# Optimization experiments

Measured on AMD Instinct MI355X. Metric: run time of the kernel, lower is better.

## Reference

```python
import jax, jax.numpy as jnp
import numpy as np

B, T, DIN, DOUT = 32, 3136, 192, 384
H, QS, WS = 6, 4, 16            # heads, q_stride, window_size (post-pool)
HD = DOUT // H                   # head_dim = 64
INNER = QS * WS                  # tokens per mask unit before pooling = 64
NW = T // INNER                  # num_windows = 49
MLP_HID = 4 * DOUT
EPS = 1e-5


def layer_norm(x, w, b):
    mu = x.mean(-1, keepdims=True)
    var = ((x - mu) ** 2).mean(-1, keepdims=True)
    return (x - mu) * jax.lax.rsqrt(var + EPS) * w + b


def setup_inputs() -> dict:
    key = jax.random.key(0)
    ks = jax.random.split(key, 16)
    rn = lambda k, shp, fan: jax.random.normal(k, shp, jnp.float32) * (fan ** -0.5)
    return {
        "embeddings": jax.random.normal(ks[0], (B, T, DIN), jnp.float32),
        "norm1_w": jnp.ones((DIN,), jnp.float32),
        "norm1_b": jnp.zeros((DIN,), jnp.float32),
        "w_qkv": rn(ks[1], (3 * DOUT, DIN), DIN),
        "b_qkv": jnp.zeros((3 * DOUT,), jnp.float32),
        "w_attn_proj": rn(ks[2], (DOUT, DOUT), DOUT),
        "b_attn_proj": jnp.zeros((DOUT,), jnp.float32),
        "w_res_proj": rn(ks[3], (DOUT, DIN), DIN),
        "b_res_proj": jnp.zeros((DOUT,), jnp.float32),
        "norm2_w": jnp.ones((DOUT,), jnp.float32),
        "norm2_b": jnp.zeros((DOUT,), jnp.float32),
        "w_fc1": rn(ks[4], (MLP_HID, DOUT), DOUT),
        "b_fc1": jnp.zeros((MLP_HID,), jnp.float32),
        "w_fc2": rn(ks[5], (DOUT, MLP_HID), MLP_HID),
        "b_fc2": jnp.zeros((DOUT,), jnp.float32),
    }


def _block(embeddings, norm1_w, norm1_b, w_qkv, b_qkv, w_attn_proj, b_attn_proj,
           w_res_proj, b_res_proj, norm2_w, norm2_b, w_fc1, b_fc1, w_fc2, b_fc2):
    x = layer_norm(embeddings, norm1_w, norm1_b)                 # [B,T,DIN]

    # residual path: project then do_pool (max over q_stride groups)
    res = x @ w_res_proj.T + b_res_proj                          # [B,T,DOUT]
    res = res.reshape(B, QS, T // QS, DOUT).max(axis=1)          # [B,T/QS,DOUT]

    # mask-unit attention
    qkv = x @ w_qkv.T + b_qkv                                    # [B,T,3*DOUT]
    qkv = qkv.reshape(B, INNER, NW, 3, H, HD)
    qkv = jnp.transpose(qkv, (3, 0, 4, 2, 1, 5))                 # [3,B,H,NW,INNER,HD]
    q, k, v = qkv[0], qkv[1], qkv[2]
    q = q.reshape(B, H, NW, QS, WS, HD).max(axis=3)              # q-pool -> [B,H,NW,WS,HD]
    scale = HD ** -0.5
    attn = jax.nn.softmax(jnp.einsum("bhwqd,bhwkd->bhwqk", q * scale, k), axis=-1)
    out = jnp.einsum("bhwqk,bhwkd->bhwqd", attn, v)              # [B,H,NW,WS,HD]
    out = jnp.transpose(out, (0, 3, 2, 1, 4)).reshape(B, WS * NW, DOUT)
    out = out @ w_attn_proj.T + b_attn_proj

    emb = res + out
    h = layer_norm(emb, norm2_w, norm2_b)
    h = jax.nn.gelu(h @ w_fc1.T + b_fc1, approximate=False)
    emb = emb + (h @ w_fc2.T + b_fc2)
    return emb, attn


def reference(embeddings, norm1_w, norm1_b, w_qkv, b_qkv, w_attn_proj, b_attn_proj,
              w_res_proj, b_res_proj, norm2_w, norm2_b, w_fc1, b_fc1, w_fc2, b_fc2):
    return _block(embeddings, norm1_w, norm1_b, w_qkv, b_qkv, w_attn_proj, b_attn_proj,
                  w_res_proj, b_res_proj, norm2_w, norm2_b, w_fc1, b_fc1, w_fc2, b_fc2)
```

## Files before the change

### kernel.cpp

```cpp
#include <hip/hip_runtime.h>
#include <stdint.h>

typedef __bf16 bf16_t;
typedef __attribute__((ext_vector_type(8))) __bf16 bf16x8;
typedef __attribute__((ext_vector_type(4))) __bf16 bf16x4;
typedef __attribute__((ext_vector_type(4))) float f32x4;

#define NB_ 32
#define NT_ 3136
#define DIN_ 192
#define DOUT_ 384
#define NH_ 6
#define HD_ 64
#define NW_ 49
#define WSZ_ 16
#define TP_ 784
#define MLP_ 1536

__device__ __forceinline__ f32x4 mfma16(bf16x8 a, bf16x8 b, f32x4 c) {
  return __builtin_amdgcn_mfma_f32_16x16x32_bf16(a, b, c, 0, 0, 0);
}

__device__ __forceinline__ void gload_lds16(const bf16_t* g, bf16_t* l) {
  __builtin_amdgcn_global_load_lds(
      (const __attribute__((address_space(1))) void*)((const void*)g),
      (__attribute__((address_space(3))) void*)l, 16, 0, 0);
}

__device__ __forceinline__ float gelu_tanh(float v) {
  const float t2 = 1.5957691216f * (v + 0.044715f * v * v * v);
  return v * (1.f - 1.f / (1.f + __expf(t2)));
}

__global__ void cvt_kernel(const float* __restrict__ s0, const float* __restrict__ s1,
                           const float* __restrict__ s2, const float* __restrict__ s3,
                           const float* __restrict__ s4, bf16_t* __restrict__ d0,
                           bf16_t* __restrict__ d1, bf16_t* __restrict__ d2,
                           bf16_t* __restrict__ d3, bf16_t* __restrict__ d4) {
  const int b = blockIdx.x;
  const float* s; bf16_t* d; long off;
  if (b < 108)      { s = s0; d = d0; off = (long)b * 2048; }
  else if (b < 144) { s = s1; d = d1; off = (long)(b - 108) * 2048; }
  else if (b < 216) { s = s2; d = d2; off = (long)(b - 144) * 2048; }
  else if (b < 504) { s = s3; d = d3; off = (long)(b - 216) * 2048; }
  else              { s = s4; d = d4; off = (long)(b - 504) * 2048; }
  off += (long)threadIdx.x * 8;
  const float4 a = *(const float4*)(s + off);
  const float4 c = *(const float4*)(s + off + 4);
  bf16x8 o;
  o[0] = (bf16_t)a.x; o[1] = (bf16_t)a.y; o[2] = (bf16_t)a.z; o[3] = (bf16_t)a.w;
  o[4] = (bf16_t)c.x; o[5] = (bf16_t)c.y; o[6] = (bf16_t)c.z; o[7] = (bf16_t)c.w;
  *(bf16x8*)(d + off) = o;
}

template <int D>
__global__ void ln_f32_kernel(const float* __restrict__ in, const float* __restrict__ w,
                              const float* __restrict__ bvec, bf16_t* __restrict__ out) {
  const int row = blockIdx.x * 4 + (threadIdx.x >> 6);
  const int lane = threadIdx.x & 63;
  constexpr int PER = D / 64;
  const float* x = in + (long)row * D;
  float v[PER];
  float s = 0.f;
#pragma unroll
  for (int i = 0; i < PER; i++) { v[i] = x[lane * PER + i]; s += v[i]; }
#pragma unroll
  for (int off = 1; off < 64; off <<= 1) s += __shfl_xor(s, off);
  const float mu = s * (1.f / D);
  float s2 = 0.f;
#pragma unroll
  for (int i = 0; i < PER; i++) { const float d = v[i] - mu; s2 += d * d; }
#pragma unroll
  for (int off = 1; off < 64; off <<= 1) s2 += __shfl_xor(s2, off);
  const float rstd = rsqrtf(s2 * (1.f / D) + 1e-5f);
  bf16_t* o = out + (long)row * D;
#pragma unroll
  for (int i = 0; i < PER; i++) {
    const int c = lane * PER + i;
    o[c] = (bf16_t)((v[i] - mu) * rstd * w[c] + bvec[c]);
  }
}

template <int D>
__global__ void ln_bf16_kernel(const bf16_t* __restrict__ in, const float* __restrict__ w,
                               const float* __restrict__ bvec, bf16_t* __restrict__ out) {
  const int row = blockIdx.x * 4 + (threadIdx.x >> 6);
  const int lane = threadIdx.x & 63;
  constexpr int PER = D / 64;
  const bf16_t* x = in + (long)row * D;
  float v[PER];
  float s = 0.f;
#pragma unroll
  for (int i = 0; i < PER; i++) { v[i] = (float)x[lane * PER + i]; s += v[i]; }
#pragma unroll
  for (int off = 1; off < 64; off <<= 1) s += __shfl_xor(s, off);
  const float mu = s * (1.f / D);
  float s2 = 0.f;
#pragma unroll
  for (int i = 0; i < PER; i++) { const float d = v[i] - mu; s2 += d * d; }
#pragma unroll
  for (int off = 1; off < 64; off <<= 1) s2 += __shfl_xor(s2, off);
  const float rstd = rsqrtf(s2 * (1.f / D) + 1e-5f);
  bf16_t* o = out + (long)row * D;
#pragma unroll
  for (int i = 0; i < PER; i++) {
    const int c = lane * PER + i;
    o[c] = (bf16_t)((v[i] - mu) * rstd * w[c] + bvec[c]);
  }
}

template <int ACT, int POOL>
__global__ __launch_bounds__(512, 4) void gemm8(
    const bf16_t* __restrict__ A, const bf16_t* __restrict__ W,
    const float* __restrict__ bias, bf16_t* __restrict__ C,
    int M, int N, int K) {
  __shared__ __align__(16) char AsB[256 * 128];
  __shared__ __align__(16) char WsB[128 * 128];

  const int nwg = gridDim.x;
  const int q = nwg >> 3, rm = nwg & 7;
  const int xcd = blockIdx.x & 7, idx = blockIdx.x >> 3;
  const int wg = (xcd < rm ? xcd * (q + 1) : rm * (q + 1) + (xcd - rm) * q) + idx;

  const int nbn = N >> 7;
  const int bmi = wg / nbn;
  const int bni = wg - bmi * nbn;
  const int m0 = bmi << 8, n0 = bni << 7;
  const int tid = threadIdx.x;
  const int lane = tid & 63;
  const int wid = tid >> 6;
  const int wr = (wid >> 1) * 64, wc = (wid & 1) * 64;
  const int l15 = lane & 15;
  const int lkb = (lane >> 4) << 4;
  const int srow = tid >> 3;
  const int scolsw = ((tid & 7) << 3) ^ ((srow & 7) << 3);
  const int swzr = (l15 & 7) << 4;

  f32x4 acc[4][4];
  const f32x4 zero = {0.f, 0.f, 0.f, 0.f};
#pragma unroll
  for (int i = 0; i < 4; i++)
#pragma unroll
    for (int j = 0; j < 4; j++) acc[i][j] = zero;

  long arow[4];
#pragma unroll
  for (int p = 0; p < 4; p++) {
    const int m = m0 + p * 64 + srow;
    if constexpr (POOL) {
      const int b = m / NT_;
      const int mm = m - b * NT_;
      arow[p] = (long)b * NT_ + (mm & 3) * TP_ + (mm >> 2);
    } else {
      arow[p] = m;
    }
  }
  long wrow[2];
#pragma unroll
  for (int p = 0; p < 2; p++) wrow[p] = (long)(n0 + p * 64 + srow);

  for (int k0 = 0; k0 < K; k0 += 64) {
    __syncthreads();
#pragma unroll
    for (int p = 0; p < 4; p++)
      gload_lds16(A + arow[p] * K + k0 + scolsw, (bf16_t*)(AsB + p * 8192 + tid * 16));
#pragma unroll
    for (int p = 0; p < 2; p++)
      gload_lds16(W + wrow[p] * K + k0 + scolsw, (bf16_t*)(WsB + p * 8192 + tid * 16));
    __syncthreads();
#pragma unroll
    for (int kk = 0; kk < 2; kk++) {
      bf16x8 af[4], wf[4];
#pragma unroll
      for (int i = 0; i < 4; i++)
        af[i] = *(const bf16x8*)(AsB + (wr + i * 16 + l15) * 128 + ((kk * 64 + lkb) ^ swzr));
#pragma unroll
      for (int j = 0; j < 4; j++)
        wf[j] = *(const bf16x8*)(WsB + (wc + j * 16 + l15) * 128 + ((kk * 64 + lkb) ^ swzr));
#pragma unroll
      for (int i = 0; i < 4; i++)
#pragma unroll
        for (int j = 0; j < 4; j++) {
          if constexpr (POOL) acc[i][j] = mfma16(af[i], wf[j], acc[i][j]);
          else                acc[i][j] = mfma16(wf[j], af[i], acc[i][j]);
        }
    }
  }

  const int rg = (lane >> 4) * 4;
  if constexpr (POOL) {
#pragma unroll
    for (int j = 0; j < 4; j++) {
      const int gn = n0 + wc + j * 16 + l15;
      const float bv = bias[gn];
#pragma unroll
      for (int i = 0; i < 4; i++) {
        const float v = fmaxf(fmaxf(acc[i][j][0], acc[i][j][1]),
                              fmaxf(acc[i][j][2], acc[i][j][3])) + bv;
        const long pm = (long)((m0 + wr + i * 16 + rg) >> 2);
        C[pm * N + gn] = (bf16_t)v;
      }
    }
  } else {
    __syncthreads();
    char* scr = AsB + wid * 4096;
#pragma unroll
    for (int i = 0; i < 4; i++) {
#pragma unroll
      for (int j = 0; j < 4; j++)
        *(f32x4*)(scr + l15 * 256 + ((((j * 16 + rg) << 2)) ^ ((l15 & 7) << 4))) = acc[i][j];
#pragma unroll
      for (int k = 0; k < 4; k++) {
        const int rl = k * 4 + (lane >> 4);
        const int cb = (lane & 15) << 4;
        const f32x4 v = *(const f32x4*)(scr + rl * 256 + (cb ^ ((rl & 7) << 4)));
        const long gm = m0 + wr + i * 16 + rl;
        const int gn = n0 + wc + ((lane & 15) << 2);
        const float4 bv = *(const float4*)(bias + gn);
        float vv[4] = {v[0] + bv.x, v[1] + bv.y, v[2] + bv.z, v[3] + bv.w};
        if constexpr (ACT == 1) {
#pragma unroll
          for (int r = 0; r < 4; r++) vv[r] = gelu_tanh(vv[r]);
        }
        bf16x4 o;
#pragma unroll
        for (int r = 0; r < 4; r++) o[r] = (bf16_t)vv[r];
        *(bf16x4*)(C + gm * N + gn) = o;
      }
    }
  }
}

template <int HASRES, int OF32, int RF32>
__global__ __launch_bounds__(256) void gemm_t(
    const bf16_t* __restrict__ A, const bf16_t* __restrict__ W,
    const float* __restrict__ bias, const void* __restrict__ resv,
    void* __restrict__ Cv, int M, int N, int K) {
  constexpr int BM = 64;
  constexpr int PA = BM / 32;
  constexpr int ABYTES = BM * 128;
  constexpr int BUFSZ = ABYTES + 128 * 128;
  __shared__ __align__(16) char LDSB[2 * BUFSZ];

  const int nwg = gridDim.x;
  const int q = nwg >> 3, rm = nwg & 7;
  const int xcd = blockIdx.x & 7, idx = blockIdx.x >> 3;
  const int wg = (xcd < rm ? xcd * (q + 1) : rm * (q + 1) + (xcd - rm) * q) + idx;

  const int nbn = N >> 7;
  const int bmi = wg / nbn;
  const int bni = wg - bmi * nbn;
  const int m0 = bmi * BM, n0 = bni << 7;
  const int tid = threadIdx.x;
  const int lane = tid & 63;
  const int wid = tid >> 6;
  const int wr = (wid >> 1) * 32, wc = (wid & 1) * 64;
  const int l15 = lane & 15;
  const int lkb = (lane >> 4) << 4;
  const int srow = tid >> 3;
  const int scolsw = ((tid & 7) << 3) ^ ((srow & 7) << 3);
  const int swzr = (l15 & 7) << 4;

  f32x4 acc[PA][4];
  const f32x4 zero = {0.f, 0.f, 0.f, 0.f};
#pragma unroll
  for (int i = 0; i < PA; i++)
#pragma unroll
    for (int j = 0; j < 4; j++) acc[i][j] = zero;

  long arow[PA];
#pragma unroll
  for (int p = 0; p < PA; p++) arow[p] = m0 + srow + p * 32;
  long wrow[4];
#pragma unroll
  for (int p = 0; p < 4; p++) wrow[p] = (long)(n0 + srow + p * 32);

  auto stage = [&](int buf, int k0) {
    char* base = LDSB + buf * BUFSZ;
#pragma unroll
    for (int p = 0; p < PA; p++)
      gload_lds16(A + arow[p] * K + k0 + scolsw, (bf16_t*)(base + p * 4096 + tid * 16));
#pragma unroll
    for (int p = 0; p < 4; p++)
      gload_lds16(W + wrow[p] * K + k0 + scolsw,
                  (bf16_t*)(base + ABYTES + p * 4096 + tid * 16));
  };

  const int nt = K >> 6;
  stage(0, 0);
  int cur = 0;
  for (int t = 0; t < nt; t++) {
    __syncthreads();
    if (t + 1 < nt) stage(cur ^ 1, (t + 1) << 6);
    const char* base = LDSB + cur * BUFSZ;
#pragma unroll
    for (int kk = 0; kk < 2; kk++) {
      bf16x8 af[PA], wf[4];
#pragma unroll
      for (int i = 0; i < PA; i++)
        af[i] = *(const bf16x8*)(base + (wr + i * 16 + l15) * 128 + ((kk * 64 + lkb) ^ swzr));
#pragma unroll
      for (int j = 0; j < 4; j++)
        wf[j] = *(const bf16x8*)(base + ABYTES + (wc + j * 16 + l15) * 128 +
                                 ((kk * 64 + lkb) ^ swzr));
#pragma unroll
      for (int i = 0; i < PA; i++)
#pragma unroll
        for (int j = 0; j < 4; j++) acc[i][j] = mfma16(wf[j], af[i], acc[i][j]);
    }
    cur ^= 1;
  }

  __syncthreads();
  char* scr = LDSB + wid * 8192;
  const int rg = (lane >> 4) * 4;
#pragma unroll
  for (int i = 0; i < PA; i++) {
    const int ml = i * 16 + l15;
#pragma unroll
    for (int j = 0; j < 4; j++)
      *(f32x4*)(scr + ml * 256 + ((((j * 16 + rg) << 2)) ^ ((ml & 7) << 4))) = acc[i][j];
  }
#pragma unroll
  for (int k = 0; k < 8; k++) {
    const int rl = k * 4 + (lane >> 4);
    const int cb = (lane & 15) << 4;
    const f32x4 v = *(const f32x4*)(scr + rl * 256 + (cb ^ ((rl & 7) << 4)));
    const long gm = m0 + wr + rl;
    const int gn = n0 + wc + ((lane & 15) << 2);
    const float4 bv = *(const float4*)(bias + gn);
    float vv[4] = {v[0] + bv.x, v[1] + bv.y, v[2] + bv.z, v[3] + bv.w};
    if constexpr (HASRES) {
      if constexpr (RF32) {
        const float4 rv = *(const float4*)((const float*)resv + gm * N + gn);
        vv[0] += rv.x; vv[1] += rv.y; vv[2] += rv.z; vv[3] += rv.w;
      } else {
        const bf16x4 rv = *(const bf16x4*)((const bf16_t*)resv + gm * N + gn);
#pragma unroll
        for (int r = 0; r < 4; r++) vv[r] += (float)rv[r];
      }
    }
    if constexpr (OF32) {
      float4 o = {vv[0], vv[1], vv[2], vv[3]};
      *(float4*)((float*)Cv + gm * N + gn) = o;
    } else {
      bf16x4 o;
#pragma unroll
      for (int r = 0; r < 4; r++) o[r] = (bf16_t)vv[r];
      *(bf16x4*)((bf16_t*)Cv + gm * N + gn) = o;
    }
  }
}

__global__ __launch_bounds__(384) void qkv_attn_kernel(
    const bf16_t* __restrict__ x, const bf16_t* __restrict__ Wqkv,
    const float* __restrict__ bq, float* __restrict__ prob,
    bf16_t* __restrict__ obuf) {
  __shared__ __align__(16) char As[64 * 384];
  __shared__ __align__(16) char Qs[6][2048];
  __shared__ __align__(16) char Kb[6][4096];
  const int b = blockIdx.x / NW_;
  const int w = blockIdx.x - b * NW_;
  const int tid = threadIdx.x;
  const int lane = tid & 63;
  const int h = tid >> 6;
  const int l15 = lane & 15;
  const int lk8 = (lane >> 4) * 8;
  const int lkb = (lane >> 4) << 4;
  const int rg = (lane >> 4) * 4;
  const f32x4 zero = {0.f, 0.f, 0.f, 0.f};

#pragma unroll
  for (int i = 0; i < 4; i++) {
    const int row = i * 16 + tid / 24;
    const int cb = ((tid % 24) * 16) ^ ((row & 7) << 4);
    gload_lds16(x + ((long)b * NT_ + (long)row * NW_ + w) * DIN_ + cb / 2,
                (bf16_t*)(As + i * 6144 + tid * 16));
  }
  __syncthreads();

  char* Qw = Qs[h];
  char* Bw = Kb[h];
  auto gemm_part = [&](int which, f32x4 (&acc)[4][4]) {
#pragma unroll
    for (int i = 0; i < 4; i++)
#pragma unroll
      for (int j = 0; j < 4; j++) acc[i][j] = zero;
#pragma unroll
    for (int j = 0; j < 4; j++) {
      const bf16_t* wrow = Wqkv + (long)(which * DOUT_ + h * HD_ + j * 16 + l15) * DIN_;
      bf16x8 wf[6];
#pragma unroll
      for (int ks = 0; ks < 6; ks++)
        wf[ks] = *(const bf16x8*)(wrow + ks * 32 + lk8);
#pragma unroll
      for (int ks = 0; ks < 6; ks++) {
#pragma unroll
        for (int i = 0; i < 4; i++) {
          const int mr = i * 16 + l15;
          const bf16x8 af = *(const bf16x8*)(As + mr * 384 +
                                             ((ks * 64 + lkb) ^ ((mr & 7) << 4)));
          acc[i][j] = mfma16(af, wf[ks], acc[i][j]);
        }
      }
    }
  };

  f32x4 acc[4][4];
  gemm_part(0, acc);
#pragma unroll
  for (int j = 0; j < 4; j++) {
    const float bb = bq[h * HD_ + j * 16 + l15];
#pragma unroll
    for (int r = 0; r < 4; r++) {
      const float v = (fmaxf(fmaxf(acc[0][j][r], acc[1][j][r]),
                             fmaxf(acc[2][j][r], acc[3][j][r])) + bb) * 0.125f;
      const int row = rg + r;
      *(bf16_t*)(Qw + row * 128 + (((j * 16 + l15) * 2) ^ ((row & 7) << 4))) = (bf16_t)v;
    }
  }
  bf16x8 aq[2];
#pragma unroll
  for (int kc = 0; kc < 2; kc++)
    aq[kc] = *(const bf16x8*)(Qw + l15 * 128 + ((kc * 64 + lkb) ^ ((l15 & 7) << 4)));

  gemm_part(1, acc);
#pragma unroll
  for (int j = 0; j < 4; j++) {
    const float bb = bq[DOUT_ + h * HD_ + j * 16 + l15];
#pragma unroll
    for (int i = 0; i < 4; i++)
#pragma unroll
      for (int r = 0; r < 4; r++) acc[i][j][r] += bb;
  }
  f32x4 s4[4];
#pragma unroll
  for (int nc = 0; nc < 4; nc++) s4[nc] = zero;
#pragma unroll
  for (int t = 0; t < 2; t++) {
#pragma unroll
    for (int i2 = 0; i2 < 2; i2++) {
      const int i = t * 2 + i2;
#pragma unroll
      for (int j = 0; j < 4; j++)
#pragma unroll
        for (int r = 0; r < 4; r++) {
          const int tokh = i2 * 16 + rg + r;
          *(bf16_t*)(Bw + tokh * 128 + (((j * 16 + l15) * 2) ^ ((tokh & 7) << 4))) =
              (bf16_t)acc[i][j][r];
        }
    }
#pragma unroll
    for (int nch = 0; nch < 2; nch++) {
      const int nc = t * 2 + nch;
      const int tokh = nch * 16 + l15;
#pragma unroll
      for (int kc = 0; kc < 2; kc++) {
        const bf16x8 bk = *(const bf16x8*)(Bw + tokh * 128 +
                                           ((kc * 64 + lkb) ^ ((tokh & 7) << 4)));
        s4[nc] = mfma16(aq[kc], bk, s4[nc]);
      }
    }
  }

#pragma unroll
  for (int r = 0; r < 4; r++) {
    float mx = fmaxf(fmaxf(s4[0][r], s4[1][r]), fmaxf(s4[2][r], s4[3][r]));
#pragma unroll
    for (int off = 1; off < 16; off <<= 1) mx = fmaxf(mx, __shfl_xor(mx, off));
    float sm = 0.f;
#pragma unroll
    for (int nc = 0; nc < 4; nc++) {
      const float p = __expf(s4[nc][r] - mx);
      s4[nc][r] = p;
      sm += p;
    }
#pragma unroll
    for (int off = 1; off < 16; off <<= 1) sm += __shfl_xor(sm, off);
    const float inv = 1.f / sm;
#pragma unroll
    for (int nc = 0; nc < 4; nc++) s4[nc][r] *= inv;
  }

  float* aout = prob + (long)((b * NH_ + h) * NW_ + w) * (WSZ_ * 64);
#pragma unroll
  for (int nc = 0; nc < 4; nc++) {
#pragma unroll
    for (int r = 0; r < 4; r++) {
      const int row = rg + r, col = nc * 16 + l15;
      aout[row * 64 + col] = s4[nc][r];
      *(bf16_t*)(Qw + row * 128 + ((col * 2) ^ ((row & 7) << 4))) = (bf16_t)s4[nc][r];
    }
  }
  bf16x8 ap[2];
#pragma unroll
  for (int kc = 0; kc < 2; kc++)
    ap[kc] = *(const bf16x8*)(Qw + l15 * 128 + ((kc * 64 + lkb) ^ ((l15 & 7) << 4)));

  gemm_part(2, acc);
#pragma unroll
  for (int j = 0; j < 4; j++) {
    const float bb = bq[2 * DOUT_ + h * HD_ + j * 16 + l15];
#pragma unroll
    for (int i = 0; i < 4; i++)
#pragma unroll
      for (int r = 0; r < 4; r++) acc[i][j][r] += bb;
  }
  f32x4 o4[4];
#pragma unroll
  for (int nc = 0; nc < 4; nc++) o4[nc] = zero;
#pragma unroll
  for (int t = 0; t < 2; t++) {
#pragma unroll
    for (int i2 = 0; i2 < 2; i2++) {
      const int i = t * 2 + i2;
#pragma unroll
      for (int j = 0; j < 4; j++)
#pragma unroll
        for (int r = 0; r < 4; r++) {
          const int tokh = i2 * 16 + rg + r;
          *(bf16_t*)(Bw + tokh * 128 + (((j * 16 + l15) * 2) ^ ((tokh & 7) << 4))) =
              (bf16_t)acc[i][j][r];
        }
    }
#pragma unroll
    for (int nc = 0; nc < 4; nc++) {
      bf16x8 bv;
#pragma unroll
      for (int e = 0; e < 8; e++) {
        const int tokh = lk8 + e;
        bv[e] = *(const bf16_t*)(Bw + tokh * 128 +
                                 (((nc * 16 + l15) * 2) ^ ((tokh & 7) << 4)));
      }
      o4[nc] = mfma16(ap[t], bv, o4[nc]);
    }
  }

#pragma unroll
  for (int nc = 0; nc < 4; nc++) {
#pragma unroll
    for (int r = 0; r < 4; r++) {
      const int row = rg + r;
      *(bf16_t*)(Qw + row * 128 + (((nc * 16 + l15) * 2) ^ ((row & 7) << 4))) =
          (bf16_t)o4[nc][r];
    }
  }
  bf16_t* ob = obuf + (long)b * TP_ * DOUT_ + h * HD_;
#pragma unroll
  for (int p = 0; p < 2; p++) {
    const int row = lane >> 2;
    const int cb = p * 64 + (lane & 3) * 16;
    const bf16x8 t = *(const bf16x8*)(Qw + row * 128 + (cb ^ ((row & 7) << 4)));
    *(bf16x8*)(ob + (long)(row * NW_ + w) * DOUT_ + cb / 2) = t;
  }
}

extern "C" void kernel_launch(void* const* d_in, const int* in_sizes, int n_in,
                              void* d_out, int out_size, void* d_ws, size_t ws_size,
                              hipStream_t stream) {
  const float* emb   = (const float*)d_in[0];
  const float* n1w   = (const float*)d_in[1];
  const float* n1b   = (const float*)d_in[2];
  const float* wqkv  = (const float*)d_in[3];
  const float* bqkv  = (const float*)d_in[4];
  const float* wproj = (const float*)d_in[5];
  const float* bproj = (const float*)d_in[6];
  const float* wres  = (const float*)d_in[7];
  const float* bres  = (const float*)d_in[8];
  const float* n2w   = (const float*)d_in[9];
  const float* n2b   = (const float*)d_in[10];
  const float* wfc1  = (const float*)d_in[11];
  const float* bfc1  = (const float*)d_in[12];
  const float* wfc2  = (const float*)d_in[13];
  const float* bfc2  = (const float*)d_in[14];
  float* out = (float*)d_out;

  const int BT = NB_ * NT_;
  const int BTP = NB_ * TP_;

  char* wsb = (char*)d_ws;
  bf16_t* x    = (bf16_t*)(wsb);
  bf16_t* h1   = (bf16_t*)(wsb);
  bf16_t* obuf = (bf16_t*)(wsb + 57802752L);
  bf16_t* resp = (bf16_t*)(wsb + 77070336L);
  bf16_t* h0   = resp;
  bf16_t* emb1 = (bf16_t*)(wsb + 96337920L);
  bf16_t* wbqkv = (bf16_t*)(wsb + 115605504L);
  bf16_t* wbres = wbqkv + 221184L;
  bf16_t* wbproj = wbres + 73728L;
  bf16_t* wbfc1 = wbproj + 147456L;
  bf16_t* wbfc2 = wbfc1 + 589824L;
  float*  prob = out + 9633792L;

  cvt_kernel<<<792, 256, 0, stream>>>(wqkv, wres, wproj, wfc1, wfc2,
                                      wbqkv, wbres, wbproj, wbfc1, wbfc2);
  ln_f32_kernel<DIN_><<<BT / 4, 256, 0, stream>>>(emb, n1w, n1b, x);
  gemm8<0, 1><<<(BT / 256) * (DOUT_ / 128), 512, 0, stream>>>(
      x, wbres, bres, resp, BT, DOUT_, DIN_);
  qkv_attn_kernel<<<NB_ * NW_, 384, 0, stream>>>(x, wbqkv, bqkv, prob, obuf);
  gemm_t<1, 0, 0><<<(BTP / 64) * (DOUT_ / 128), 256, 0, stream>>>(
      obuf, wbproj, bproj, resp, emb1, BTP, DOUT_, DOUT_);
  ln_bf16_kernel<DOUT_><<<BTP / 4, 256, 0, stream>>>(emb1, n2w, n2b, h0);
  gemm8<1, 0><<<(BTP / 256) * (MLP_ / 128), 512, 0, stream>>>(
      h0, wbfc1, bfc1, h1, BTP, MLP_, DOUT_);
  gemm_t<1, 1, 0><<<(BTP / 64) * (DOUT_ / 128), 256, 0, stream>>>(
      h1, wbfc2, bfc2, emb1, out, BTP, DOUT_, MLP_);
}
```

Before: 312.4 us.

## Process two batch elements per attention block to reuse QKV weight fragments

The fused QKV+attention kernel now handles two batch items per block for the same window. Each weight fragment loaded from global memory feeds MFMAs for both items, which halves weight traffic per output and halves the grid size. The cost is double the accumulator registers (acc0/acc1 of 16 f32x4 each), larger LDS (about 96KB per block), and a launch-bounds hint of 2 blocks per CU that may force spills. The smaller grid of 784 blocks also lowers parallelism.

```diff
diff --git a/kernel.cpp b/kernel.cpp
--- a/kernel.cpp
+++ b/kernel.cpp
@@ -352,15 +352,16 @@
   }
 }
 
-__global__ __launch_bounds__(384) void qkv_attn_kernel(
+__global__ __launch_bounds__(384, 2) void qkv_attn_kernel(
     const bf16_t* __restrict__ x, const bf16_t* __restrict__ Wqkv,
     const float* __restrict__ bq, float* __restrict__ prob,
     bf16_t* __restrict__ obuf) {
-  __shared__ __align__(16) char As[64 * 384];
-  __shared__ __align__(16) char Qs[6][2048];
+  __shared__ __align__(16) char As[2 * 24576];
+  __shared__ __align__(16) char Qs[6][4096];
   __shared__ __align__(16) char Kb[6][4096];
-  const int b = blockIdx.x / NW_;
-  const int w = blockIdx.x - b * NW_;
+  const int bp = blockIdx.x / NW_;
+  const int w = blockIdx.x - bp * NW_;
+  const int b0 = bp * 2;
   const int tid = threadIdx.x;
   const int lane = tid & 63;
   const int h = tid >> 6;
@@ -369,190 +370,212 @@
   const int lkb = (lane >> 4) << 4;
   const int rg = (lane >> 4) * 4;
   const f32x4 zero = {0.f, 0.f, 0.f, 0.f};
-
-#pragma unroll
-  for (int i = 0; i < 4; i++) {
-    const int row = i * 16 + tid / 24;
-    const int cb = ((tid % 24) * 16) ^ ((row & 7) << 4);
-    gload_lds16(x + ((long)b * NT_ + (long)row * NW_ + w) * DIN_ + cb / 2,
-                (bf16_t*)(As + i * 6144 + tid * 16));
-  }
-  __syncthreads();
-
   char* Qw = Qs[h];
   char* Bw = Kb[h];
-  auto gemm_part = [&](int which, f32x4 (&acc)[4][4]) {
+
+#pragma unroll
+  for (int u = 0; u < 8; u++) {
+    const int bi = u >> 2;
+    const int row = (u & 3) * 16 + tid / 24;
+    const int cb = ((tid % 24) * 16) ^ ((row & 7) << 4);
+    gload_lds16(x + ((long)(b0 + bi) * NT_ + (long)row * NW_ + w) * DIN_ + cb / 2,
+                (bf16_t*)(As + bi * 24576 + (u & 3) * 6144 + tid * 16));
+  }
+  __syncthreads();
+
+  auto afrag = [&](int bi, int mr, int ks) {
+    return *(const bf16x8*)(As + bi * 24576 + mr * 384 +
+                            ((ks * 64 + lkb) ^ ((mr & 7) << 4)));
+  };
+
+  f32x4 acc0[4][4], acc1[4][4];
+  auto gemm2 = [&](int which) {
 #pragma unroll
     for (int i = 0; i < 4; i++)
 #pragma unroll
-      for (int j = 0; j < 4; j++) acc[i][j] = zero;
+      for (int j = 0; j < 4; j++) { acc0[i][j] = zero; acc1[i][j] = zero; }
 #pragma unroll
     for (int j = 0; j < 4; j++) {
       const bf16_t* wrow = Wqkv + (long)(which * DOUT_ + h * HD_ + j * 16 + l15) * DIN_;
       bf16x8 wf[6];
 #pragma unroll
-      for (int ks = 0; ks < 6; ks++)
-        wf[ks] = *(const bf16x8*)(wrow + ks * 32 + lk8);
+      for (int ks = 0; ks < 6; ks++) wf[ks] = *(const bf16x8*)(wrow + ks * 32 + lk8);
 #pragma unroll
       for (int ks = 0; ks < 6; ks++) {
 #pragma unroll
         for (int i = 0; i < 4; i++) {
           const int mr = i * 16 + l15;
-          const bf16x8 af = *(const bf16x8*)(As + mr * 384 +
-                                             ((ks * 64 + lkb) ^ ((mr & 7) << 4)));
-          acc[i][j] = mfma16(af, wf[ks], acc[i][j]);
+          acc0[i][j] = mfma16(afrag(0, mr, ks), wf[ks], acc0[i][j]);
+          acc1[i][j] = mfma16(afrag(1, mr, ks), wf[ks], acc1[i][j]);
         }
       }
     }
   };
 
-  f32x4 acc[4][4];
-  gemm_part(0, acc);
-#pragma unroll
-  for (int j = 0; j < 4; j++) {
-    const float bb = bq[h * HD_ + j * 16 + l15];
+  gemm2(0);
+  auto qpool = [&](f32x4 (&A)[4][4], int bi) {
+#pragma unroll
+    for (int j = 0; j < 4; j++) {
+      const float bb = bq[h * HD_ + j * 16 + l15];
+#pragma unroll
+      for (int r = 0; r < 4; r++) {
+        const float v = (fmaxf(fmaxf(A[0][j][r], A[1][j][r]),
+                               fmaxf(A[2][j][r], A[3][j][r])) + bb) * 0.125f;
+        const int row = rg + r;
+        *(bf16_t*)(Qw + bi * 2048 + row * 128 +
+                   (((j * 16 + l15) * 2) ^ ((row & 7) << 4))) = (bf16_t)v;
+      }
+    }
+  };
+  qpool(acc0, 0);
+  qpool(acc1, 1);
+  bf16x8 aq0[2], aq1[2];
+#pragma unroll
+  for (int kc = 0; kc < 2; kc++) {
+    aq0[kc] = *(const bf16x8*)(Qw + l15 * 128 + ((kc * 64 + lkb) ^ ((l15 & 7) << 4)));
+    aq1[kc] = *(const bf16x8*)(Qw + 2048 + l15 * 128 + ((kc * 64 + lkb) ^ ((l15 & 7) << 4)));
+  }
+
+  gemm2(1);
+  auto addbias = [&](f32x4 (&A)[4][4], int base) {
+#pragma unroll
+    for (int j = 0; j < 4; j++) {
+      const float bb = bq[base + h * HD_ + j * 16 + l15];
+#pragma unroll
+      for (int i = 0; i < 4; i++)
+#pragma unroll
+        for (int r = 0; r < 4; r++) A[i][j][r] += bb;
+    }
+  };
+  addbias(acc0, DOUT_);
+  addbias(acc1, DOUT_);
+  f32x4 s40[4], s41[4];
+  auto sgemm = [&](f32x4 (&A)[4][4], bf16x8 (&aq)[2], f32x4 (&s4)[4]) {
+#pragma unroll
+    for (int nc = 0; nc < 4; nc++) s4[nc] = zero;
+#pragma unroll
+    for (int t = 0; t < 2; t++) {
+#pragma unroll
+      for (int i2 = 0; i2 < 2; i2++) {
+        const int i = t * 2 + i2;
+#pragma unroll
+        for (int j = 0; j < 4; j++)
+#pragma unroll
+          for (int r = 0; r < 4; r++) {
+            const int tokh = i2 * 16 + rg + r;
+            *(bf16_t*)(Bw + tokh * 128 + (((j * 16 + l15) * 2) ^ ((tokh & 7) << 4))) =
+                (bf16_t)A[i][j][r];
+          }
+      }
+#pragma unroll
+      for (int nch = 0; nch < 2; nch++) {
+        const int nc = t * 2 + nch;
+        const int tokh = nch * 16 + l15;
+#pragma unroll
+        for (int kc = 0; kc < 2; kc++) {
+          const bf16x8 bk = *(const bf16x8*)(Bw + tokh * 128 +
+                                             ((kc * 64 + lkb) ^ ((tokh & 7) << 4)));
+          s4[nc] = mfma16(aq[kc], bk, s4[nc]);
+        }
+      }
+    }
+  };
+  sgemm(acc0, aq0, s40);
+  sgemm(acc1, aq1, s41);
+
+  auto smax = [&](f32x4 (&s4)[4], int bglob, int bi) {
 #pragma unroll
     for (int r = 0; r < 4; r++) {
-      const float v = (fmaxf(fmaxf(acc[0][j][r], acc[1][j][r]),
-                             fmaxf(acc[2][j][r], acc[3][j][r])) + bb) * 0.125f;
-      const int row = rg + r;
-      *(bf16_t*)(Qw + row * 128 + (((j * 16 + l15) * 2) ^ ((row & 7) << 4))) = (bf16_t)v;
-    }
-  }
-  bf16x8 aq[2];
-#pragma unroll
-  for (int kc = 0; kc < 2; kc++)
-    aq[kc] = *(const bf16x8*)(Qw + l15 * 128 + ((kc * 64 + lkb) ^ ((l15 & 7) << 4)));
-
-  gemm_part(1, acc);
-#pragma unroll
-  for (int j = 0; j < 4; j++) {
-    const float bb = bq[DOUT_ + h * HD_ + j * 16 + l15];
-#pragma unroll
-    for (int i = 0; i < 4; i++)
-#pragma unroll
-      for (int r = 0; r < 4; r++) acc[i][j][r] += bb;
-  }
-  f32x4 s4[4];
-#pragma unroll
-  for (int nc = 0; nc < 4; nc++) s4[nc] = zero;
-#pragma unroll
-  for (int t = 0; t < 2; t++) {
-#pragma unroll
-    for (int i2 = 0; i2 < 2; i2++) {
-      const int i = t * 2 + i2;
-#pragma unroll
-      for (int j = 0; j < 4; j++)
-#pragma unroll
-        for (int r = 0; r < 4; r++) {
-          const int tokh = i2 * 16 + rg + r;
-          *(bf16_t*)(Bw + tokh * 128 + (((j * 16 + l15) * 2) ^ ((tokh & 7) << 4))) =
-              (bf16_t)acc[i][j][r];
+      float mx = fmaxf(fmaxf(s4[0][r], s4[1][r]), fmaxf(s4[2][r], s4[3][r]));
+#pragma unroll
+      for (int off = 1; off < 16; off <<= 1) mx = fmaxf(mx, __shfl_xor(mx, off));
+      float sm = 0.f;
+#pragma unroll
+      for (int nc = 0; nc < 4; nc++) {
+        const float p = __expf(s4[nc][r] - mx);
+        s4[nc][r] = p;
+        sm += p;
+      }
+#pragma unroll
+      for (int off = 1; off < 16; off <<= 1) sm += __shfl_xor(sm, off);
+      const float inv = 1.f / sm;
+#pragma unroll
+      for (int nc = 0; nc < 4; nc++) s4[nc][r] *= inv;
+    }
+    float* aout = prob + (long)((bglob * NH_ + h) * NW_ + w) * (WSZ_ * 64);
+#pragma unroll
+    for (int nc = 0; nc < 4; nc++) {
+#pragma unroll
+      for (int r = 0; r < 4; r++) {
+        const int row = rg + r, col = nc * 16 + l15;
+        aout[row * 64 + col] = s4[nc][r];
+        *(bf16_t*)(Qw + bi * 2048 + row * 128 + ((col * 2) ^ ((row & 7) << 4))) =
+            (bf16_t)s4[nc][r];
+      }
+    }
+  };
+  smax(s40, b0, 0);
+  smax(s41, b0 + 1, 1);
+  bf16x8 ap0[2], ap1[2];
+#pragma unroll
+  for (int kc = 0; kc < 2; kc++) {
+    ap0[kc] = *(const bf16x8*)(Qw + l15 * 128 + ((kc * 64 + lkb) ^ ((l15 & 7) << 4)));
+    ap1[kc] = *(const bf16x8*)(Qw + 2048 + l15 * 128 + ((kc * 64 + lkb) ^ ((l15 & 7) << 4)));
+  }
+
+  gemm2(2);
+  addbias(acc0, 2 * DOUT_);
+  addbias(acc1, 2 * DOUT_);
+  auto pv = [&](f32x4 (&A)[4][4], bf16x8 (&ap)[2], int bglob, int bi) {
+    f32x4 o4[4];
+#pragma unroll
+    for (int nc = 0; nc < 4; nc++) o4[nc] = zero;
+#pragma unroll
+    for (int t = 0; t < 2; t++) {
+#pragma unroll
+      for (int i2 = 0; i2 < 2; i2++) {
+        const int i = t * 2 + i2;
+#pragma unroll
+        for (int j = 0; j < 4; j++)
+#pragma unroll
+          for (int r = 0; r < 4; r++) {
+            const int tokh = i2 * 16 + rg + r;
+            *(bf16_t*)(Bw + tokh * 128 + (((j * 16 + l15) * 2) ^ ((tokh & 7) << 4))) =
+                (bf16_t)A[i][j][r];
+          }
+      }
+#pragma unroll
+      for (int nc = 0; nc < 4; nc++) {
+        bf16x8 bv;
+#pragma unroll
+        for (int e = 0; e < 8; e++) {
+          const int tokh = lk8 + e;
+          bv[e] = *(const bf16_t*)(Bw + tokh * 128 +
+                                   (((nc * 16 + l15) * 2) ^ ((tokh & 7) << 4)));
         }
-    }
-#pragma unroll
-    for (int nch = 0; nch < 2; nch++) {
-      const int nc = t * 2 + nch;
-      const int tokh = nch * 16 + l15;
-#pragma unroll
-      for (int kc = 0; kc < 2; kc++) {
-        const bf16x8 bk = *(const bf16x8*)(Bw + tokh * 128 +
-                                           ((kc * 64 + lkb) ^ ((tokh & 7) << 4)));
-        s4[nc] = mfma16(aq[kc], bk, s4[nc]);
-      }
-    }
-  }
-
-#pragma unroll
-  for (int r = 0; r < 4; r++) {
-    float mx = fmaxf(fmaxf(s4[0][r], s4[1][r]), fmaxf(s4[2][r], s4[3][r]));
-#pragma unroll
-    for (int off = 1; off < 16; off <<= 1) mx = fmaxf(mx, __shfl_xor(mx, off));
-    float sm = 0.f;
+        o4[nc] = mfma16(ap[t], bv, o4[nc]);
+      }
+    }
 #pragma unroll
     for (int nc = 0; nc < 4; nc++) {
-      const float p = __expf(s4[nc][r] - mx);
-      s4[nc][r] = p;
-      sm += p;
-    }
-#pragma unroll
-    for (int off = 1; off < 16; off <<= 1) sm += __shfl_xor(sm, off);
-    const float inv = 1.f / sm;
-#pragma unroll
-    for (int nc = 0; nc < 4; nc++) s4[nc][r] *= inv;
-  }
-
-  float* aout = prob + (long)((b * NH_ + h) * NW_ + w) * (WSZ_ * 64);
-#pragma unroll
-  for (int nc = 0; nc < 4; nc++) {
-#pragma unroll
-    for (int r = 0; r < 4; r++) {
-      const int row = rg + r, col = nc * 16 + l15;
-      aout[row * 64 + col] = s4[nc][r];
-      *(bf16_t*)(Qw + row * 128 + ((col * 2) ^ ((row & 7) << 4))) = (bf16_t)s4[nc][r];
-    }
-  }
-  bf16x8 ap[2];
-#pragma unroll
-  for (int kc = 0; kc < 2; kc++)
-    ap[kc] = *(const bf16x8*)(Qw + l15 * 128 + ((kc * 64 + lkb) ^ ((l15 & 7) << 4)));
-
-  gemm_part(2, acc);
-#pragma unroll
-  for (int j = 0; j < 4; j++) {
-    const float bb = bq[2 * DOUT_ + h * HD_ + j * 16 + l15];
-#pragma unroll
-    for (int i = 0; i < 4; i++)
-#pragma unroll
-      for (int r = 0; r < 4; r++) acc[i][j][r] += bb;
-  }
-  f32x4 o4[4];
-#pragma unroll
-  for (int nc = 0; nc < 4; nc++) o4[nc] = zero;
-#pragma unroll
-  for (int t = 0; t < 2; t++) {
-#pragma unroll
-    for (int i2 = 0; i2 < 2; i2++) {
-      const int i = t * 2 + i2;
-#pragma unroll
-      for (int j = 0; j < 4; j++)
-#pragma unroll
-        for (int r = 0; r < 4; r++) {
-          const int tokh = i2 * 16 + rg + r;
-          *(bf16_t*)(Bw + tokh * 128 + (((j * 16 + l15) * 2) ^ ((tokh & 7) << 4))) =
-              (bf16_t)acc[i][j][r];
-        }
-    }
-#pragma unroll
-    for (int nc = 0; nc < 4; nc++) {
-      bf16x8 bv;
-#pragma unroll
-      for (int e = 0; e < 8; e++) {
-        const int tokh = lk8 + e;
-        bv[e] = *(const bf16_t*)(Bw + tokh * 128 +
-                                 (((nc * 16 + l15) * 2) ^ ((tokh & 7) << 4)));
-      }
-      o4[nc] = mfma16(ap[t], bv, o4[nc]);
-    }
-  }
-
-#pragma unroll
-  for (int nc = 0; nc < 4; nc++) {
-#pragma unroll
-    for (int r = 0; r < 4; r++) {
-      const int row = rg + r;
-      *(bf16_t*)(Qw + row * 128 + (((nc * 16 + l15) * 2) ^ ((row & 7) << 4))) =
-          (bf16_t)o4[nc][r];
-    }
-  }
-  bf16_t* ob = obuf + (long)b * TP_ * DOUT_ + h * HD_;
-#pragma unroll
-  for (int p = 0; p < 2; p++) {
-    const int row = lane >> 2;
-    const int cb = p * 64 + (lane & 3) * 16;
-    const bf16x8 t = *(const bf16x8*)(Qw + row * 128 + (cb ^ ((row & 7) << 4)));
-    *(bf16x8*)(ob + (long)(row * NW_ + w) * DOUT_ + cb / 2) = t;
-  }
+#pragma unroll
+      for (int r = 0; r < 4; r++) {
+        const int row = rg + r;
+        *(bf16_t*)(Qw + bi * 2048 + row * 128 +
+                   (((nc * 16 + l15) * 2) ^ ((row & 7) << 4))) = (bf16_t)o4[nc][r];
+      }
+    }
+    bf16_t* ob = obuf + (long)bglob * TP_ * DOUT_ + h * HD_;
+#pragma unroll
+    for (int p = 0; p < 2; p++) {
+      const int row = lane >> 2;
+      const int cb = p * 64 + (lane & 3) * 16;
+      const bf16x8 t = *(const bf16x8*)(Qw + bi * 2048 + row * 128 + (cb ^ ((row & 7) << 4)));
+      *(bf16x8*)(ob + (long)(row * NW_ + w) * DOUT_ + cb / 2) = t;
+    }
+  };
+  pv(acc0, ap0, b0, 0);
+  pv(acc1, ap1, b0 + 1, 1);
 }
 
 extern "C" void kernel_launch(void* const* d_in, const int* in_sizes, int n_in,
@@ -597,7 +620,7 @@
   ln_f32_kernel<DIN_><<<BT / 4, 256, 0, stream>>>(emb, n1w, n1b, x);
   gemm8<0, 1><<<(BT / 256) * (DOUT_ / 128), 512, 0, stream>>>(
       x, wbres, bres, resp, BT, DOUT_, DIN_);
-  qkv_attn_kernel<<<NB_ * NW_, 384, 0, stream>>>(x, wbqkv, bqkv, prob, obuf);
+  qkv_attn_kernel<<<(NB_ / 2) * NW_, 384, 0, stream>>>(x, wbqkv, bqkv, prob, obuf);
   gemm_t<1, 0, 0><<<(BTP / 64) * (DOUT_ / 128), 256, 0, stream>>>(
       obuf, wbproj, bproj, resp, emb1, BTP, DOUT_, DOUT_);
   ln_bf16_kernel<DOUT_><<<BTP / 4, 256, 0, stream>>>(emb1, n2w, n2b, h0);
```

After: 472.2 us. 1.51x slower.
